# Performance work log

Measured on AMD Instinct MI355X. Metric: run time of the kernel, lower is better.

Reference implementation:

```python
import jax, jax.numpy as jnp
import numpy as np

IN_FEATURES = 4096
PADDED = 4096               # padded_dim == in_features -> no crop
K_HALF = PADDED // 2 + 1    # 2049
K = 1024                    # truncation: only first K half-spectrum coeffs active
BATCH = 8192


def setup_inputs() -> dict:
    key = jax.random.key(0)
    k1, k2, k3, k4 = jax.random.split(key, 4)
    x = jax.random.normal(k1, (BATCH, IN_FEATURES), dtype=jnp.float32)
    w_real = jax.random.normal(k2, (K_HALF,), dtype=jnp.float32) * 0.1
    w_imag = jax.random.normal(k3, (K_HALF,), dtype=jnp.float32) * 0.1
    # DC and Nyquist bins must be real (Hermitian spectrum of a real filter)
    w_imag = w_imag.at[0].set(0.0).at[-1].set(0.0)
    bias = jax.random.normal(k4, (), dtype=jnp.float32) * 0.1
    return {"x": x, "w_real": w_real, "w_imag": w_imag, "bias": bias}


def _fft_full(w_real, w_imag):
    # K-truncated half spectrum -> full Hermitian-symmetric spectrum (PADDED even)
    mask = (jnp.arange(K_HALF) < K).astype(w_real.dtype)
    half = w_real * mask + 1j * (w_imag * mask)            # (K_HALF,) complex
    nyq = half[-1].real[None].astype(half.dtype)           # real Nyquist bin
    full = jnp.concatenate([half[:-1], nyq, jnp.conj(half[1:-1])[::-1]])
    return full                                            # (PADDED,) complex


def reference(x, w_real, w_imag, bias):
    # in_features == padded_dim: no padding, no crop
    fft_full = _fft_full(w_real, w_imag)
    Xf = jnp.fft.fft(x, axis=-1, norm="ortho")             # (B, PADDED) complex
    y = jnp.fft.ifft(Xf * fft_full, axis=-1, norm="ortho").real
    return y + bias                                        # scalar bias (vector_bias=False)
```

## Files before the change

kernel.cpp:

```cpp
#include <hip/hip_runtime.h>

#define NT 256


template<bool INV>
__device__ __forceinline__ void dft16(float* vr, float* vi) {
    constexpr float C1 = 0.9238795325112867f;
    constexpr float S1 = 0.3826834323650898f;
    constexpr float HF = 0.7071067811865476f;
    const float WR[10] = {1.f,  C1,  HF,  S1, 0.f, 0.f, -HF, 0.f, 0.f, -C1};
    const float WI[10] = {0.f, -S1, -HF, -C1, -1.f, 0.f, -HF, 0.f, 0.f,  S1};

    float ar[16], ai[16];
    #pragma unroll
    for (int jl = 0; jl < 4; ++jl) {
        float x0r = vr[jl],      x0i = vi[jl];
        float x1r = vr[jl + 4],  x1i = vi[jl + 4];
        float x2r = vr[jl + 8],  x2i = vi[jl + 8];
        float x3r = vr[jl + 12], x3i = vi[jl + 12];
        float t0r = x0r + x2r, t0i = x0i + x2i;
        float t1r = x0r - x2r, t1i = x0i - x2i;
        float t2r = x1r + x3r, t2i = x1i + x3i;
        float t3r = x1r - x3r, t3i = x1i - x3i;
        ar[jl]     = t0r + t2r;  ai[jl]     = t0i + t2i;
        ar[jl + 8] = t0r - t2r;  ai[jl + 8] = t0i - t2i;
        if (!INV) {
            ar[jl + 4]  = t1r + t3i;  ai[jl + 4]  = t1i - t3r;
            ar[jl + 12] = t1r - t3i;  ai[jl + 12] = t1i + t3r;
        } else {
            ar[jl + 4]  = t1r - t3i;  ai[jl + 4]  = t1i + t3r;
            ar[jl + 12] = t1r + t3i;  ai[jl + 12] = t1i - t3r;
        }
    }
    #pragma unroll
    for (int k4 = 1; k4 < 4; ++k4) {
        #pragma unroll
        for (int jl = 1; jl < 4; ++jl) {
            const int e = jl * k4;
            float wr = WR[e];
            float wi = INV ? -WI[e] : WI[e];
            const int id = jl + 4 * k4;
            float xr = ar[id], xi = ai[id];
            ar[id] = xr * wr - xi * wi;
            ai[id] = xr * wi + xi * wr;
        }
    }
    #pragma unroll
    for (int k4 = 0; k4 < 4; ++k4) {
        float x0r = ar[4*k4 + 0], x0i = ai[4*k4 + 0];
        float x1r = ar[4*k4 + 1], x1i = ai[4*k4 + 1];
        float x2r = ar[4*k4 + 2], x2i = ai[4*k4 + 2];
        float x3r = ar[4*k4 + 3], x3i = ai[4*k4 + 3];
        float t0r = x0r + x2r, t0i = x0i + x2i;
        float t1r = x0r - x2r, t1i = x0i - x2i;
        float t2r = x1r + x3r, t2i = x1i + x3i;
        float t3r = x1r - x3r, t3i = x1i - x3i;
        vr[k4]     = t0r + t2r;  vi[k4]     = t0i + t2i;
        vr[k4 + 8] = t0r - t2r;  vi[k4 + 8] = t0i - t2i;
        if (!INV) {
            vr[k4 + 4]  = t1r + t3i;  vi[k4 + 4]  = t1i - t3r;
            vr[k4 + 12] = t1r - t3i;  vi[k4 + 12] = t1i + t3r;
        } else {
            vr[k4 + 4]  = t1r - t3i;  vi[k4 + 4]  = t1i + t3r;
            vr[k4 + 12] = t1r + t3i;  vi[k4 + 12] = t1i - t3r;
        }
    }
}

__device__ __forceinline__ void apply_tw_powers(float* vr, float* vi, float wr, float wi) {
    const float w2r = wr * wr - wi * wi;
    const float w2i = 2.0f * wr * wi;
    float aor = wr,  aoi = wi;
    float aer = w2r, aei = w2i;
    #pragma unroll
    for (int e = 1; e < 16; e += 2) {
        { float xr = vr[e], xi = vi[e];
          vr[e] = xr * aor - xi * aoi;
          vi[e] = xr * aoi + xi * aor; }
        if (e + 1 < 16) {
            float xr = vr[e + 1], xi = vi[e + 1];
            vr[e + 1] = xr * aer - xi * aei;
            vi[e + 1] = xr * aei + xi * aer;
        }
        if (e + 2 < 16) {
            float nr = aor * w2r - aoi * w2i, ni = aor * w2i + aoi * w2r;
            aor = nr; aoi = ni;
            nr = aer * w2r - aei * w2i; ni = aer * w2i + aei * w2r;
            aer = nr; aei = ni;
        }
    }
}

__global__ __launch_bounds__(NT, 4) void spectral_circulant_r16v5(
    const float* __restrict__ x,
    const float* __restrict__ w_real,
    const float* __restrict__ w_imag,
    const float* __restrict__ bias_p,
    float* __restrict__ out)
{
    __shared__ __align__(16) float2 lds[4096];

    const int t   = threadIdx.x;
    const int blk = blockIdx.x;

    float vr[16], vi[16];

    const float* __restrict__ xa = x + (size_t)(2 * blk) * 4096;
    const float* __restrict__ xb = xa + 4096;
    #pragma unroll
    for (int j = 0; j < 16; ++j) {
        vr[j] = xa[(j << 8) + t];
        vi[j] = xb[(j << 8) + t];
    }

    dft16<false>(vr, vi);
    float sA, cA;
    __sincosf((float)t * -1.5339807878856412e-3f, &sA, &cA);
    apply_tw_powers(vr, vi, cA, sA);

    {
        const int tswz = t ^ ((t >> 3) & 0xE);
        #pragma unroll
        for (int a = 0; a < 16; ++a)
            lds[(a << 8) + tswz] = make_float2(vr[a], vi[a]);
    }
    __syncthreads();

    const int ax = t >> 4;
    const int m2 = t & 15;

    int swzbase[8];
    #pragma unroll
    for (int c = 0; c < 8; ++c)
        swzbase[c] = (ax << 8) + (m2 ^ (c << 1));

    #pragma unroll
    for (int q = 0; q < 16; ++q) {
        float2 v = lds[swzbase[q & 7] + (q << 4)];
        vr[q] = v.x; vi[q] = v.y;
    }

    dft16<false>(vr, vi);
    float sB, cB;
    __sincosf((float)m2 * -2.454369260617026e-2f, &sB, &cB);
    apply_tw_powers(vr, vi, cB, sB);

    #pragma unroll
    for (int b = 0; b < 16; ++b)
        lds[swzbase[b & 7] + (b << 4)] = make_float2(vr[b], vi[b]);
    __builtin_amdgcn_wave_barrier();

    const int c2 = (m2 & 7) << 1;
    const float2* __restrict__ pbase = &lds[(ax << 8) + (m2 << 4)];
    #pragma unroll
    for (int m = 0; m < 16; m += 2) {
        float4 v = *(const float4*)&pbase[m ^ c2];
        vr[m] = v.x;     vi[m] = v.y;
        vr[m + 1] = v.z; vi[m + 1] = v.w;
    }

    dft16<false>(vr, vi);

    {
        const int c = (m2 << 4) | ax;
        const float sc = 1.0f / 4096.0f;
        #pragma unroll
        for (int r3 = 0; r3 < 4; ++r3) {
            const int k = (r3 << 8) + c;
            float hr = w_real[k] * sc;
            float hi = w_imag[k] * sc;
            float xr = vr[r3], xi = vi[r3];
            vr[r3] = xr * hr - xi * hi;
            vi[r3] = xr * hi + xi * hr;
        }
        #pragma unroll
        for (int r3 = 4; r3 < 12; ++r3) {
            vr[r3] = 0.0f; vi[r3] = 0.0f;
        }
        {
            const int idx = 1024 - c;
            const float m = (c > 0) ? sc : 0.0f;
            float hr = w_real[idx] * m;
            float hi = -w_imag[idx] * m;
            float xr = vr[12], xi = vi[12];
            vr[12] = xr * hr - xi * hi;
            vi[12] = xr * hi + xi * hr;
        }
        #pragma unroll
        for (int r3 = 13; r3 < 16; ++r3) {
            const int idx = ((16 - r3) << 8) - c;
            float hr = w_real[idx] * sc;
            float hi = -w_imag[idx] * sc;
            float xr = vr[r3], xi = vi[r3];
            vr[r3] = xr * hr - xi * hi;
            vi[r3] = xr * hi + xi * hr;
        }
    }


    dft16<true>(vr, vi);

    {
        float2* __restrict__ pw = &lds[(ax << 8) + (m2 << 4)];
        #pragma unroll
        for (int m = 0; m < 16; m += 2)
            *(float4*)&pw[m ^ c2] = make_float4(vr[m], vi[m], vr[m + 1], vi[m + 1]);
    }
    __builtin_amdgcn_wave_barrier();

    #pragma unroll
    for (int b = 0; b < 16; ++b) {
        float2 v = lds[swzbase[b & 7] + (b << 4)];
        vr[b] = v.x; vi[b] = v.y;
    }

    apply_tw_powers(vr, vi, cB, -sB);
    dft16<true>(vr, vi);

    #pragma unroll
    for (int q = 0; q < 16; ++q)
        lds[swzbase[q & 7] + (q << 4)] = make_float2(vr[q], vi[q]);
    __syncthreads();

    {
        const int tswz = t ^ ((t >> 3) & 0xE);
        #pragma unroll
        for (int a = 0; a < 16; ++a) {
            float2 v = lds[(a << 8) + tswz];
            vr[a] = v.x; vi[a] = v.y;
        }
    }

    apply_tw_powers(vr, vi, cA, -sA);
    dft16<true>(vr, vi);

    const float bv = bias_p[0];
    float* __restrict__ oa = out + (size_t)(2 * blk) * 4096;
    float* __restrict__ ob = oa + 4096;
    #pragma unroll
    for (int j = 0; j < 16; ++j) {
        __builtin_nontemporal_store(vr[j] + bv, &oa[(j << 8) + t]);
        __builtin_nontemporal_store(vi[j] + bv, &ob[(j << 8) + t]);
    }
}

extern "C" void kernel_launch(void* const* d_in, const int* in_sizes, int n_in,
                              void* d_out, int out_size, void* d_ws, size_t ws_size,
                              hipStream_t stream) {
    (void)in_sizes; (void)n_in; (void)d_ws; (void)ws_size; (void)out_size;
    const float* x      = (const float*)d_in[0];
    const float* w_real = (const float*)d_in[1];
    const float* w_imag = (const float*)d_in[2];
    const float* bias   = (const float*)d_in[3];
    float* out = (float*)d_out;

    spectral_circulant_r16v5<<<8192 / 2, NT, 0, stream>>>(x, w_real, w_imag, bias, out);
}
```

Before: 242.0 us.

## Process four rows per block as two complex FFTs per thread

Each block now handles four input rows, packed as two complex 4096-point FFTs (P and Q) per thread instead of one. Twiddle factors, weight loads and sincos work are shared across both transforms, and each thread has more independent instruction streams to hide latency. The cost is double the LDS per block (64 KB), more registers, and a lower launch-bounds occupancy target of 2 blocks per CU. The grid is halved to match.

```diff
diff --git a/kernel.cpp b/kernel.cpp
--- a/kernel.cpp
+++ b/kernel.cpp
@@ -67,20 +67,28 @@
     }
 }
 
-__device__ __forceinline__ void apply_tw_powers(float* vr, float* vi, float wr, float wi) {
+__device__ __forceinline__ void apply_tw_dual(float* vrP, float* viP,
+                                              float* vrQ, float* viQ,
+                                              float wr, float wi) {
     const float w2r = wr * wr - wi * wi;
     const float w2i = 2.0f * wr * wi;
     float aor = wr,  aoi = wi;
     float aer = w2r, aei = w2i;
     #pragma unroll
     for (int e = 1; e < 16; e += 2) {
-        { float xr = vr[e], xi = vi[e];
-          vr[e] = xr * aor - xi * aoi;
-          vi[e] = xr * aoi + xi * aor; }
+        { float xr = vrP[e], xi = viP[e];
+          vrP[e] = xr * aor - xi * aoi;
+          viP[e] = xr * aoi + xi * aor; }
+        { float xr = vrQ[e], xi = viQ[e];
+          vrQ[e] = xr * aor - xi * aoi;
+          viQ[e] = xr * aoi + xi * aor; }
         if (e + 1 < 16) {
-            float xr = vr[e + 1], xi = vi[e + 1];
-            vr[e + 1] = xr * aer - xi * aei;
-            vi[e + 1] = xr * aei + xi * aer;
+            { float xr = vrP[e + 1], xi = viP[e + 1];
+              vrP[e + 1] = xr * aer - xi * aei;
+              viP[e + 1] = xr * aei + xi * aer; }
+            { float xr = vrQ[e + 1], xi = viQ[e + 1];
+              vrQ[e + 1] = xr * aer - xi * aei;
+              viQ[e + 1] = xr * aei + xi * aer; }
         }
         if (e + 2 < 16) {
             float nr = aor * w2r - aoi * w2i, ni = aor * w2i + aoi * w2r;
@@ -91,38 +99,49 @@
     }
 }
 
-__global__ __launch_bounds__(NT, 4) void spectral_circulant_r16v5(
+__device__ __forceinline__ void cmul(float& r, float& i, float hr, float hi) {
+    float xr = r, xi = i;
+    r = xr * hr - xi * hi;
+    i = xr * hi + xi * hr;
+}
+
+__global__ __launch_bounds__(NT, 2) void spectral_circulant_r16v6(
     const float* __restrict__ x,
     const float* __restrict__ w_real,
     const float* __restrict__ w_imag,
     const float* __restrict__ bias_p,
     float* __restrict__ out)
 {
-    __shared__ __align__(16) float2 lds[4096];
+    __shared__ __align__(16) float2 lds[8192];
 
     const int t   = threadIdx.x;
     const int blk = blockIdx.x;
 
-    float vr[16], vi[16];
-
-    const float* __restrict__ xa = x + (size_t)(2 * blk) * 4096;
-    const float* __restrict__ xb = xa + 4096;
+    float vrP[16], viP[16], vrQ[16], viQ[16];
+
+    const float* __restrict__ xa = x + (size_t)(4 * blk) * 4096;
     #pragma unroll
     for (int j = 0; j < 16; ++j) {
-        vr[j] = xa[(j << 8) + t];
-        vi[j] = xb[(j << 8) + t];
-    }
-
-    dft16<false>(vr, vi);
+        const int o = (j << 8) + t;
+        vrP[j] = xa[o];
+        viP[j] = xa[o + 4096];
+        vrQ[j] = xa[o + 8192];
+        viQ[j] = xa[o + 12288];
+    }
+
+    dft16<false>(vrP, viP);
+    dft16<false>(vrQ, viQ);
     float sA, cA;
     __sincosf((float)t * -1.5339807878856412e-3f, &sA, &cA);
-    apply_tw_powers(vr, vi, cA, sA);
+    apply_tw_dual(vrP, viP, vrQ, viQ, cA, sA);
 
     {
         const int tswz = t ^ ((t >> 3) & 0xE);
         #pragma unroll
-        for (int a = 0; a < 16; ++a)
-            lds[(a << 8) + tswz] = make_float2(vr[a], vi[a]);
+        for (int a = 0; a < 16; ++a) {
+            lds[(a << 8) + tswz]        = make_float2(vrP[a], viP[a]);
+            lds[(a << 8) + tswz + 4096] = make_float2(vrQ[a], viQ[a]);
+        }
     }
     __syncthreads();
 
@@ -136,30 +155,39 @@
 
     #pragma unroll
     for (int q = 0; q < 16; ++q) {
-        float2 v = lds[swzbase[q & 7] + (q << 4)];
-        vr[q] = v.x; vi[q] = v.y;
-    }
-
-    dft16<false>(vr, vi);
+        float2 vP = lds[swzbase[q & 7] + (q << 4)];
+        float2 vQ = lds[swzbase[q & 7] + (q << 4) + 4096];
+        vrP[q] = vP.x; viP[q] = vP.y;
+        vrQ[q] = vQ.x; viQ[q] = vQ.y;
+    }
+
+    dft16<false>(vrP, viP);
+    dft16<false>(vrQ, viQ);
     float sB, cB;
     __sincosf((float)m2 * -2.454369260617026e-2f, &sB, &cB);
-    apply_tw_powers(vr, vi, cB, sB);
-
-    #pragma unroll
-    for (int b = 0; b < 16; ++b)
-        lds[swzbase[b & 7] + (b << 4)] = make_float2(vr[b], vi[b]);
+    apply_tw_dual(vrP, viP, vrQ, viQ, cB, sB);
+
+    #pragma unroll
+    for (int b = 0; b < 16; ++b) {
+        lds[swzbase[b & 7] + (b << 4)]        = make_float2(vrP[b], viP[b]);
+        lds[swzbase[b & 7] + (b << 4) + 4096] = make_float2(vrQ[b], viQ[b]);
+    }
     __builtin_amdgcn_wave_barrier();
 
     const int c2 = (m2 & 7) << 1;
     const float2* __restrict__ pbase = &lds[(ax << 8) + (m2 << 4)];
     #pragma unroll
     for (int m = 0; m < 16; m += 2) {
-        float4 v = *(const float4*)&pbase[m ^ c2];
-        vr[m] = v.x;     vi[m] = v.y;
-        vr[m + 1] = v.z; vi[m + 1] = v.w;
-    }
-
-    dft16<false>(vr, vi);
+        float4 vP = *(const float4*)&pbase[m ^ c2];
+        float4 vQ = *(const float4*)&pbase[(m ^ c2) + 4096];
+        vrP[m] = vP.x;     viP[m] = vP.y;
+        vrP[m + 1] = vP.z; viP[m + 1] = vP.w;
+        vrQ[m] = vQ.x;     viQ[m] = vQ.y;
+        vrQ[m + 1] = vQ.z; viQ[m + 1] = vQ.w;
+    }
+
+    dft16<false>(vrP, viP);
+    dft16<false>(vrQ, viQ);
 
     {
         const int c = (m2 << 4) | ax;
@@ -169,78 +197,89 @@
             const int k = (r3 << 8) + c;
             float hr = w_real[k] * sc;
             float hi = w_imag[k] * sc;
-            float xr = vr[r3], xi = vi[r3];
-            vr[r3] = xr * hr - xi * hi;
-            vi[r3] = xr * hi + xi * hr;
+            cmul(vrP[r3], viP[r3], hr, hi);
+            cmul(vrQ[r3], viQ[r3], hr, hi);
         }
         #pragma unroll
         for (int r3 = 4; r3 < 12; ++r3) {
-            vr[r3] = 0.0f; vi[r3] = 0.0f;
+            vrP[r3] = 0.0f; viP[r3] = 0.0f;
+            vrQ[r3] = 0.0f; viQ[r3] = 0.0f;
         }
         {
             const int idx = 1024 - c;
-            const float m = (c > 0) ? sc : 0.0f;
-            float hr = w_real[idx] * m;
-            float hi = -w_imag[idx] * m;
-            float xr = vr[12], xi = vi[12];
-            vr[12] = xr * hr - xi * hi;
-            vi[12] = xr * hi + xi * hr;
+            const float mm = (c > 0) ? sc : 0.0f;
+            float hr = w_real[idx] * mm;
+            float hi = -w_imag[idx] * mm;
+            cmul(vrP[12], viP[12], hr, hi);
+            cmul(vrQ[12], viQ[12], hr, hi);
         }
         #pragma unroll
         for (int r3 = 13; r3 < 16; ++r3) {
             const int idx = ((16 - r3) << 8) - c;
             float hr = w_real[idx] * sc;
             float hi = -w_imag[idx] * sc;
-            float xr = vr[r3], xi = vi[r3];
-            vr[r3] = xr * hr - xi * hi;
-            vi[r3] = xr * hi + xi * hr;
-        }
-    }
-
-
-    dft16<true>(vr, vi);
+            cmul(vrP[r3], viP[r3], hr, hi);
+            cmul(vrQ[r3], viQ[r3], hr, hi);
+        }
+    }
+
+
+    dft16<true>(vrP, viP);
+    dft16<true>(vrQ, viQ);
 
     {
         float2* __restrict__ pw = &lds[(ax << 8) + (m2 << 4)];
         #pragma unroll
-        for (int m = 0; m < 16; m += 2)
-            *(float4*)&pw[m ^ c2] = make_float4(vr[m], vi[m], vr[m + 1], vi[m + 1]);
+        for (int m = 0; m < 16; m += 2) {
+            *(float4*)&pw[m ^ c2]          = make_float4(vrP[m], viP[m], vrP[m + 1], viP[m + 1]);
+            *(float4*)&pw[(m ^ c2) + 4096] = make_float4(vrQ[m], viQ[m], vrQ[m + 1], viQ[m + 1]);
+        }
     }
     __builtin_amdgcn_wave_barrier();
 
     #pragma unroll
     for (int b = 0; b < 16; ++b) {
-        float2 v = lds[swzbase[b & 7] + (b << 4)];
-        vr[b] = v.x; vi[b] = v.y;
-    }
-
-    apply_tw_powers(vr, vi, cB, -sB);
-    dft16<true>(vr, vi);
-
-    #pragma unroll
-    for (int q = 0; q < 16; ++q)
-        lds[swzbase[q & 7] + (q << 4)] = make_float2(vr[q], vi[q]);
+        float2 vP = lds[swzbase[b & 7] + (b << 4)];
+        float2 vQ = lds[swzbase[b & 7] + (b << 4) + 4096];
+        vrP[b] = vP.x; viP[b] = vP.y;
+        vrQ[b] = vQ.x; viQ[b] = vQ.y;
+    }
+
+    apply_tw_dual(vrP, viP, vrQ, viQ, cB, -sB);
+    dft16<true>(vrP, viP);
+    dft16<true>(vrQ, viQ);
+
+    #pragma unroll
+    for (int q = 0; q < 16; ++q) {
+        lds[swzbase[q & 7] + (q << 4)]        = make_float2(vrP[q], viP[q]);
+        lds[swzbase[q & 7] + (q << 4) + 4096] = make_float2(vrQ[q], viQ[q]);
+    }
     __syncthreads();
 
     {
         const int tswz = t ^ ((t >> 3) & 0xE);
         #pragma unroll
         for (int a = 0; a < 16; ++a) {
-            float2 v = lds[(a << 8) + tswz];
-            vr[a] = v.x; vi[a] = v.y;
-        }
-    }
-
-    apply_tw_powers(vr, vi, cA, -sA);
-    dft16<true>(vr, vi);
+            float2 vP = lds[(a << 8) + tswz];
+            float2 vQ = lds[(a << 8) + tswz + 4096];
+            vrP[a] = vP.x; viP[a] = vP.y;
+            vrQ[a] = vQ.x; viQ[a] = vQ.y;
+        }
+    }
+
+    apply_tw_dual(vrP, viP, vrQ, viQ, cA, -sA);
+    dft16<true>(vrP, viP);
+    dft16<true>(vrQ, viQ);
 
     const float bv = bias_p[0];
-    float* __restrict__ oa = out + (size_t)(2 * blk) * 4096;
-    float* __restrict__ ob = oa + 4096;
+    float* __restrict__ oa = out + (size_t)(4 * blk) * 4096;
     #pragma unroll
     for (int j = 0; j < 16; ++j) {
-        __builtin_nontemporal_store(vr[j] + bv, &oa[(j << 8) + t]);
-        __builtin_nontemporal_store(vi[j] + bv, &ob[(j << 8) + t]);
+        const int o = (j << 8) + t;
+        __builtin_nontemporal_store(vrP[j] + bv, &oa[o]);
+        __builtin_nontemporal_store(viP[j] + bv, &oa[o + 4096]);
+        __builtin_nontemporal_store(vrQ[j] + bv, &oa[o + 8192]);
+        __builtin_nontemporal_store(viQ[j] + bv, &oa[o + 12288]);
     }
 }
 
@@ -254,5 +293,5 @@
     const float* bias   = (const float*)d_in[3];
     float* out = (float*)d_out;
 
-    spectral_circulant_r16v5<<<8192 / 2, NT, 0, stream>>>(x, w_real, w_imag, bias, out);
-}
+    spectral_circulant_r16v6<<<8192 / 4, NT, 0, stream>>>(x, w_real, w_imag, bias, out);
+}
```

Result: slower. 248.7 us (+2.8%).

## Process four rows per block using packed float2 vector arithmetic

Applied to the files above, without the earlier changes.

Each block now handles four input rows instead of two by packing two complex FFTs into v2f vector lanes. This lets the compiler use packed FP32 instructions (v_pk_fma/v_pk_mul) and halves the block count. LDS is split into separate real and imaginary arrays of v2f, doubling shared memory to 64 KB per block, and launch bounds drop to 2 blocks per CU. The gain in arithmetic throughput comes at the cost of more registers and lower occupancy, which may hurt latency hiding for this memory-bound kernel.

```diff
diff --git a/kernel.cpp b/kernel.cpp
--- a/kernel.cpp
+++ b/kernel.cpp
@@ -3,25 +3,28 @@
 #define NT 256
 
 
+typedef float v2f __attribute__((ext_vector_type(2)));
+typedef float v4f __attribute__((ext_vector_type(4)));
+
 template<bool INV>
-__device__ __forceinline__ void dft16(float* vr, float* vi) {
+__device__ __forceinline__ void dft16(v2f* vr, v2f* vi) {
     constexpr float C1 = 0.9238795325112867f;
     constexpr float S1 = 0.3826834323650898f;
     constexpr float HF = 0.7071067811865476f;
     const float WR[10] = {1.f,  C1,  HF,  S1, 0.f, 0.f, -HF, 0.f, 0.f, -C1};
     const float WI[10] = {0.f, -S1, -HF, -C1, -1.f, 0.f, -HF, 0.f, 0.f,  S1};
 
-    float ar[16], ai[16];
+    v2f ar[16], ai[16];
     #pragma unroll
     for (int jl = 0; jl < 4; ++jl) {
-        float x0r = vr[jl],      x0i = vi[jl];
-        float x1r = vr[jl + 4],  x1i = vi[jl + 4];
-        float x2r = vr[jl + 8],  x2i = vi[jl + 8];
-        float x3r = vr[jl + 12], x3i = vi[jl + 12];
-        float t0r = x0r + x2r, t0i = x0i + x2i;
-        float t1r = x0r - x2r, t1i = x0i - x2i;
-        float t2r = x1r + x3r, t2i = x1i + x3i;
-        float t3r = x1r - x3r, t3i = x1i - x3i;
+        v2f x0r = vr[jl],      x0i = vi[jl];
+        v2f x1r = vr[jl + 4],  x1i = vi[jl + 4];
+        v2f x2r = vr[jl + 8],  x2i = vi[jl + 8];
+        v2f x3r = vr[jl + 12], x3i = vi[jl + 12];
+        v2f t0r = x0r + x2r, t0i = x0i + x2i;
+        v2f t1r = x0r - x2r, t1i = x0i - x2i;
+        v2f t2r = x1r + x3r, t2i = x1i + x3i;
+        v2f t3r = x1r - x3r, t3i = x1i - x3i;
         ar[jl]     = t0r + t2r;  ai[jl]     = t0i + t2i;
         ar[jl + 8] = t0r - t2r;  ai[jl + 8] = t0i - t2i;
         if (!INV) {
@@ -37,24 +40,24 @@
         #pragma unroll
         for (int jl = 1; jl < 4; ++jl) {
             const int e = jl * k4;
-            float wr = WR[e];
-            float wi = INV ? -WI[e] : WI[e];
+            const float wr = WR[e];
+            const float wi = INV ? -WI[e] : WI[e];
             const int id = jl + 4 * k4;
-            float xr = ar[id], xi = ai[id];
+            v2f xr = ar[id], xi = ai[id];
             ar[id] = xr * wr - xi * wi;
             ai[id] = xr * wi + xi * wr;
         }
     }
     #pragma unroll
     for (int k4 = 0; k4 < 4; ++k4) {
-        float x0r = ar[4*k4 + 0], x0i = ai[4*k4 + 0];
-        float x1r = ar[4*k4 + 1], x1i = ai[4*k4 + 1];
-        float x2r = ar[4*k4 + 2], x2i = ai[4*k4 + 2];
-        float x3r = ar[4*k4 + 3], x3i = ai[4*k4 + 3];
-        float t0r = x0r + x2r, t0i = x0i + x2i;
-        float t1r = x0r - x2r, t1i = x0i - x2i;
-        float t2r = x1r + x3r, t2i = x1i + x3i;
-        float t3r = x1r - x3r, t3i = x1i - x3i;
+        v2f x0r = ar[4*k4 + 0], x0i = ai[4*k4 + 0];
+        v2f x1r = ar[4*k4 + 1], x1i = ai[4*k4 + 1];
+        v2f x2r = ar[4*k4 + 2], x2i = ai[4*k4 + 2];
+        v2f x3r = ar[4*k4 + 3], x3i = ai[4*k4 + 3];
+        v2f t0r = x0r + x2r, t0i = x0i + x2i;
+        v2f t1r = x0r - x2r, t1i = x0i - x2i;
+        v2f t2r = x1r + x3r, t2i = x1i + x3i;
+        v2f t3r = x1r - x3r, t3i = x1i - x3i;
         vr[k4]     = t0r + t2r;  vi[k4]     = t0i + t2i;
         vr[k4 + 8] = t0r - t2r;  vi[k4 + 8] = t0i - t2i;
         if (!INV) {
@@ -67,18 +70,18 @@
     }
 }
 
-__device__ __forceinline__ void apply_tw_powers(float* vr, float* vi, float wr, float wi) {
+__device__ __forceinline__ void apply_tw(v2f* vr, v2f* vi, float wr, float wi) {
     const float w2r = wr * wr - wi * wi;
     const float w2i = 2.0f * wr * wi;
     float aor = wr,  aoi = wi;
     float aer = w2r, aei = w2i;
     #pragma unroll
     for (int e = 1; e < 16; e += 2) {
-        { float xr = vr[e], xi = vi[e];
+        { v2f xr = vr[e], xi = vi[e];
           vr[e] = xr * aor - xi * aoi;
           vi[e] = xr * aoi + xi * aor; }
         if (e + 1 < 16) {
-            float xr = vr[e + 1], xi = vi[e + 1];
+            v2f xr = vr[e + 1], xi = vi[e + 1];
             vr[e + 1] = xr * aer - xi * aei;
             vi[e + 1] = xr * aei + xi * aer;
         }
@@ -91,38 +94,47 @@
     }
 }
 
-__global__ __launch_bounds__(NT, 4) void spectral_circulant_r16v5(
+__device__ __forceinline__ void cmul(v2f& r, v2f& i, float hr, float hi) {
+    v2f xr = r, xi = i;
+    r = xr * hr - xi * hi;
+    i = xr * hi + xi * hr;
+}
+
+__global__ __launch_bounds__(NT, 2) void spectral_circulant_r16v7(
     const float* __restrict__ x,
     const float* __restrict__ w_real,
     const float* __restrict__ w_imag,
     const float* __restrict__ bias_p,
     float* __restrict__ out)
 {
-    __shared__ __align__(16) float2 lds[4096];
+    __shared__ __align__(16) v2f ldsR[4096];
+    __shared__ __align__(16) v2f ldsI[4096];
 
     const int t   = threadIdx.x;
     const int blk = blockIdx.x;
 
-    float vr[16], vi[16];
-
-    const float* __restrict__ xa = x + (size_t)(2 * blk) * 4096;
-    const float* __restrict__ xb = xa + 4096;
+    v2f vr[16], vi[16];
+
+    const float* __restrict__ xa = x + (size_t)(4 * blk) * 4096;
     #pragma unroll
     for (int j = 0; j < 16; ++j) {
-        vr[j] = xa[(j << 8) + t];
-        vi[j] = xb[(j << 8) + t];
+        const int o = (j << 8) + t;
+        vr[j] = (v2f){xa[o],        xa[o + 8192]};
+        vi[j] = (v2f){xa[o + 4096], xa[o + 12288]};
     }
 
     dft16<false>(vr, vi);
     float sA, cA;
     __sincosf((float)t * -1.5339807878856412e-3f, &sA, &cA);
-    apply_tw_powers(vr, vi, cA, sA);
+    apply_tw(vr, vi, cA, sA);
 
     {
         const int tswz = t ^ ((t >> 3) & 0xE);
         #pragma unroll
-        for (int a = 0; a < 16; ++a)
-            lds[(a << 8) + tswz] = make_float2(vr[a], vi[a]);
+        for (int a = 0; a < 16; ++a) {
+            ldsR[(a << 8) + tswz] = vr[a];
+            ldsI[(a << 8) + tswz] = vi[a];
+        }
     }
     __syncthreads();
 
@@ -136,27 +148,30 @@
 
     #pragma unroll
     for (int q = 0; q < 16; ++q) {
-        float2 v = lds[swzbase[q & 7] + (q << 4)];
-        vr[q] = v.x; vi[q] = v.y;
+        vr[q] = ldsR[swzbase[q & 7] + (q << 4)];
+        vi[q] = ldsI[swzbase[q & 7] + (q << 4)];
     }
 
     dft16<false>(vr, vi);
     float sB, cB;
     __sincosf((float)m2 * -2.454369260617026e-2f, &sB, &cB);
-    apply_tw_powers(vr, vi, cB, sB);
-
-    #pragma unroll
-    for (int b = 0; b < 16; ++b)
-        lds[swzbase[b & 7] + (b << 4)] = make_float2(vr[b], vi[b]);
+    apply_tw(vr, vi, cB, sB);
+
+    #pragma unroll
+    for (int b = 0; b < 16; ++b) {
+        ldsR[swzbase[b & 7] + (b << 4)] = vr[b];
+        ldsI[swzbase[b & 7] + (b << 4)] = vi[b];
+    }
     __builtin_amdgcn_wave_barrier();
 
     const int c2 = (m2 & 7) << 1;
-    const float2* __restrict__ pbase = &lds[(ax << 8) + (m2 << 4)];
+    const int l0 = (ax << 8) + (m2 << 4);
     #pragma unroll
     for (int m = 0; m < 16; m += 2) {
-        float4 v = *(const float4*)&pbase[m ^ c2];
-        vr[m] = v.x;     vi[m] = v.y;
-        vr[m + 1] = v.z; vi[m + 1] = v.w;
+        v4f r4 = *(const v4f*)&ldsR[l0 + (m ^ c2)];
+        v4f i4 = *(const v4f*)&ldsI[l0 + (m ^ c2)];
+        vr[m] = r4.xy;  vr[m + 1] = r4.zw;
+        vi[m] = i4.xy;  vi[m + 1] = i4.zw;
     }
 
     dft16<false>(vr, vi);
@@ -167,80 +182,75 @@
         #pragma unroll
         for (int r3 = 0; r3 < 4; ++r3) {
             const int k = (r3 << 8) + c;
-            float hr = w_real[k] * sc;
-            float hi = w_imag[k] * sc;
-            float xr = vr[r3], xi = vi[r3];
-            vr[r3] = xr * hr - xi * hi;
-            vi[r3] = xr * hi + xi * hr;
+            cmul(vr[r3], vi[r3], w_real[k] * sc, w_imag[k] * sc);
         }
         #pragma unroll
         for (int r3 = 4; r3 < 12; ++r3) {
-            vr[r3] = 0.0f; vi[r3] = 0.0f;
+            vr[r3] = (v2f){0.0f, 0.0f};
+            vi[r3] = (v2f){0.0f, 0.0f};
         }
         {
             const int idx = 1024 - c;
-            const float m = (c > 0) ? sc : 0.0f;
-            float hr = w_real[idx] * m;
-            float hi = -w_imag[idx] * m;
-            float xr = vr[12], xi = vi[12];
-            vr[12] = xr * hr - xi * hi;
-            vi[12] = xr * hi + xi * hr;
+            const float mm = (c > 0) ? sc : 0.0f;
+            cmul(vr[12], vi[12], w_real[idx] * mm, -w_imag[idx] * mm);
         }
         #pragma unroll
         for (int r3 = 13; r3 < 16; ++r3) {
             const int idx = ((16 - r3) << 8) - c;
-            float hr = w_real[idx] * sc;
-            float hi = -w_imag[idx] * sc;
-            float xr = vr[r3], xi = vi[r3];
-            vr[r3] = xr * hr - xi * hi;
-            vi[r3] = xr * hi + xi * hr;
+            cmul(vr[r3], vi[r3], w_real[idx] * sc, -w_imag[idx] * sc);
         }
     }
 
 
     dft16<true>(vr, vi);
 
-    {
-        float2* __restrict__ pw = &lds[(ax << 8) + (m2 << 4)];
-        #pragma unroll
-        for (int m = 0; m < 16; m += 2)
-            *(float4*)&pw[m ^ c2] = make_float4(vr[m], vi[m], vr[m + 1], vi[m + 1]);
+    #pragma unroll
+    for (int m = 0; m < 16; m += 2) {
+        v4f r4, i4;
+        r4.xy = vr[m];  r4.zw = vr[m + 1];
+        i4.xy = vi[m];  i4.zw = vi[m + 1];
+        *(v4f*)&ldsR[l0 + (m ^ c2)] = r4;
+        *(v4f*)&ldsI[l0 + (m ^ c2)] = i4;
     }
     __builtin_amdgcn_wave_barrier();
 
     #pragma unroll
     for (int b = 0; b < 16; ++b) {
-        float2 v = lds[swzbase[b & 7] + (b << 4)];
-        vr[b] = v.x; vi[b] = v.y;
-    }
-
-    apply_tw_powers(vr, vi, cB, -sB);
+        vr[b] = ldsR[swzbase[b & 7] + (b << 4)];
+        vi[b] = ldsI[swzbase[b & 7] + (b << 4)];
+    }
+
+    apply_tw(vr, vi, cB, -sB);
     dft16<true>(vr, vi);
 
     #pragma unroll
-    for (int q = 0; q < 16; ++q)
-        lds[swzbase[q & 7] + (q << 4)] = make_float2(vr[q], vi[q]);
+    for (int q = 0; q < 16; ++q) {
+        ldsR[swzbase[q & 7] + (q << 4)] = vr[q];
+        ldsI[swzbase[q & 7] + (q << 4)] = vi[q];
+    }
     __syncthreads();
 
     {
         const int tswz = t ^ ((t >> 3) & 0xE);
         #pragma unroll
         for (int a = 0; a < 16; ++a) {
-            float2 v = lds[(a << 8) + tswz];
-            vr[a] = v.x; vi[a] = v.y;
-        }
-    }
-
-    apply_tw_powers(vr, vi, cA, -sA);
+            vr[a] = ldsR[(a << 8) + tswz];
+            vi[a] = ldsI[(a << 8) + tswz];
+        }
+    }
+
+    apply_tw(vr, vi, cA, -sA);
     dft16<true>(vr, vi);
 
     const float bv = bias_p[0];
-    float* __restrict__ oa = out + (size_t)(2 * blk) * 4096;
-    float* __restrict__ ob = oa + 4096;
+    float* __restrict__ oa = out + (size_t)(4 * blk) * 4096;
     #pragma unroll
     for (int j = 0; j < 16; ++j) {
-        __builtin_nontemporal_store(vr[j] + bv, &oa[(j << 8) + t]);
-        __builtin_nontemporal_store(vi[j] + bv, &ob[(j << 8) + t]);
+        const int o = (j << 8) + t;
+        __builtin_nontemporal_store(vr[j].x + bv, &oa[o]);
+        __builtin_nontemporal_store(vi[j].x + bv, &oa[o + 4096]);
+        __builtin_nontemporal_store(vr[j].y + bv, &oa[o + 8192]);
+        __builtin_nontemporal_store(vi[j].y + bv, &oa[o + 12288]);
     }
 }
 
@@ -254,5 +264,5 @@
     const float* bias   = (const float*)d_in[3];
     float* out = (float*)d_out;
 
-    spectral_circulant_r16v5<<<8192 / 2, NT, 0, stream>>>(x, w_real, w_imag, bias, out);
-}
+    spectral_circulant_r16v7<<<8192 / 4, NT, 0, stream>>>(x, w_real, w_imag, bias, out);
+}
```

Result: no change. 243.6 us (+0.6%).

## Process two row-pairs per block with software prefetch of the next input

Applied to the files above, without the earlier changes.

Each block now handles two pairs of rows (grid halved to 2048 blocks). The second pair's global loads are issued partway through the first pair's FFT pipeline, so they overlap with compute. Filter coefficients and twiddle seeds are loaded once per block and reused across both units. The cost is 32 extra live registers for the prefetch buffer, which may lower occupancy or cause spills under the 4-wave launch bound, and fewer blocks means less latency hiding across blocks.

```diff
diff --git a/kernel.cpp b/kernel.cpp
--- a/kernel.cpp
+++ b/kernel.cpp
@@ -91,7 +91,126 @@
     }
 }
 
-__global__ __launch_bounds__(NT, 4) void spectral_circulant_r16v5(
+template<bool PRE>
+__device__ __forceinline__ void process_unit(
+    float2* lds, const int t, const int ax, const int m2,
+    const int (&swzbase)[8], const int c2,
+    const float cA, const float sA, const float cB, const float sB,
+    const float (&hR)[8], const float (&hI)[8], const float bv,
+    float (&vr)[16], float (&vi)[16],
+    float (&pr)[16], float (&pi)[16],
+    const float* __restrict__ xnext,
+    float* __restrict__ oa)
+{
+    dft16<false>(vr, vi);
+    apply_tw_powers(vr, vi, cA, sA);
+
+    {
+        const int tswz = t ^ ((t >> 3) & 0xE);
+        #pragma unroll
+        for (int a = 0; a < 16; ++a)
+            lds[(a << 8) + tswz] = make_float2(vr[a], vi[a]);
+    }
+    __syncthreads();
+
+    #pragma unroll
+    for (int q = 0; q < 16; ++q) {
+        float2 v = lds[swzbase[q & 7] + (q << 4)];
+        vr[q] = v.x; vi[q] = v.y;
+    }
+
+    dft16<false>(vr, vi);
+    apply_tw_powers(vr, vi, cB, sB);
+
+    #pragma unroll
+    for (int b = 0; b < 16; ++b)
+        lds[swzbase[b & 7] + (b << 4)] = make_float2(vr[b], vi[b]);
+    __builtin_amdgcn_wave_barrier();
+
+    const float2* __restrict__ pbase = &lds[(ax << 8) + (m2 << 4)];
+    #pragma unroll
+    for (int m = 0; m < 16; m += 2) {
+        float4 v = *(const float4*)&pbase[m ^ c2];
+        vr[m] = v.x;     vi[m] = v.y;
+        vr[m + 1] = v.z; vi[m + 1] = v.w;
+    }
+
+    if constexpr (PRE) {
+        #pragma unroll
+        for (int j = 0; j < 16; ++j) {
+            pr[j] = xnext[(j << 8) + t];
+            pi[j] = xnext[(j << 8) + t + 4096];
+        }
+    }
+
+    dft16<false>(vr, vi);
+
+    {
+        #pragma unroll
+        for (int r3 = 0; r3 < 4; ++r3) {
+            float xr = vr[r3], xi = vi[r3];
+            vr[r3] = xr * hR[r3] - xi * hI[r3];
+            vi[r3] = xr * hI[r3] + xi * hR[r3];
+        }
+        #pragma unroll
+        for (int r3 = 4; r3 < 12; ++r3) { vr[r3] = 0.0f; vi[r3] = 0.0f; }
+        {
+            float xr = vr[12], xi = vi[12];
+            vr[12] = xr * hR[4] - xi * hI[4];
+            vi[12] = xr * hI[4] + xi * hR[4];
+        }
+        #pragma unroll
+        for (int r3 = 13; r3 < 16; ++r3) {
+            float xr = vr[r3], xi = vi[r3];
+            vr[r3] = xr * hR[r3 - 8] - xi * hI[r3 - 8];
+            vi[r3] = xr * hI[r3 - 8] + xi * hR[r3 - 8];
+        }
+    }
+
+    dft16<true>(vr, vi);
+
+    {
+        float2* __restrict__ pw = &lds[(ax << 8) + (m2 << 4)];
+        #pragma unroll
+        for (int m = 0; m < 16; m += 2)
+            *(float4*)&pw[m ^ c2] = make_float4(vr[m], vi[m], vr[m + 1], vi[m + 1]);
+    }
+    __builtin_amdgcn_wave_barrier();
+
+    #pragma unroll
+    for (int b = 0; b < 16; ++b) {
+        float2 v = lds[swzbase[b & 7] + (b << 4)];
+        vr[b] = v.x; vi[b] = v.y;
+    }
+
+    apply_tw_powers(vr, vi, cB, -sB);
+    dft16<true>(vr, vi);
+
+    #pragma unroll
+    for (int q = 0; q < 16; ++q)
+        lds[swzbase[q & 7] + (q << 4)] = make_float2(vr[q], vi[q]);
+    __syncthreads();
+
+    {
+        const int tswz = t ^ ((t >> 3) & 0xE);
+        #pragma unroll
+        for (int a = 0; a < 16; ++a) {
+            float2 v = lds[(a << 8) + tswz];
+            vr[a] = v.x; vi[a] = v.y;
+        }
+    }
+
+    apply_tw_powers(vr, vi, cA, -sA);
+    dft16<true>(vr, vi);
+
+    #pragma unroll
+    for (int j = 0; j < 16; ++j) {
+        __builtin_nontemporal_store(vr[j] + bv, &oa[(j << 8) + t]);
+        __builtin_nontemporal_store(vi[j] + bv, &oa[(j << 8) + t + 4096]);
+    }
+}
+
+__global__ __launch_bounds__(NT, 4) void spectral_circulant_r16v8(
     const float* __restrict__ x,
     const float* __restrict__ w_real,
     const float* __restrict__ w_imag,
@@ -102,146 +221,62 @@
 
     const int t   = threadIdx.x;
     const int blk = blockIdx.x;
-
-    float vr[16], vi[16];
-
-    const float* __restrict__ xa = x + (size_t)(2 * blk) * 4096;
-    const float* __restrict__ xb = xa + 4096;
-    #pragma unroll
-    for (int j = 0; j < 16; ++j) {
-        vr[j] = xa[(j << 8) + t];
-        vi[j] = xb[(j << 8) + t];
-    }
-
-    dft16<false>(vr, vi);
-    float sA, cA;
-    __sincosf((float)t * -1.5339807878856412e-3f, &sA, &cA);
-    apply_tw_powers(vr, vi, cA, sA);
-
-    {
-        const int tswz = t ^ ((t >> 3) & 0xE);
-        #pragma unroll
-        for (int a = 0; a < 16; ++a)
-            lds[(a << 8) + tswz] = make_float2(vr[a], vi[a]);
-    }
-    __syncthreads();
-
-    const int ax = t >> 4;
-    const int m2 = t & 15;
+    const int ax  = t >> 4;
+    const int m2  = t & 15;
 
     int swzbase[8];
     #pragma unroll
     for (int c = 0; c < 8; ++c)
         swzbase[c] = (ax << 8) + (m2 ^ (c << 1));
-
-    #pragma unroll
-    for (int q = 0; q < 16; ++q) {
-        float2 v = lds[swzbase[q & 7] + (q << 4)];
-        vr[q] = v.x; vi[q] = v.y;
-    }
-
-    dft16<false>(vr, vi);
-    float sB, cB;
+    const int c2 = (m2 & 7) << 1;
+
+    float sA, cA, sB, cB;
+    __sincosf((float)t  * -1.5339807878856412e-3f, &sA, &cA);
     __sincosf((float)m2 * -2.454369260617026e-2f, &sB, &cB);
-    apply_tw_powers(vr, vi, cB, sB);
-
-    #pragma unroll
-    for (int b = 0; b < 16; ++b)
-        lds[swzbase[b & 7] + (b << 4)] = make_float2(vr[b], vi[b]);
-    __builtin_amdgcn_wave_barrier();
-
-    const int c2 = (m2 & 7) << 1;
-    const float2* __restrict__ pbase = &lds[(ax << 8) + (m2 << 4)];
-    #pragma unroll
-    for (int m = 0; m < 16; m += 2) {
-        float4 v = *(const float4*)&pbase[m ^ c2];
-        vr[m] = v.x;     vi[m] = v.y;
-        vr[m + 1] = v.z; vi[m + 1] = v.w;
-    }
-
-    dft16<false>(vr, vi);
-
+
+    float hR[8], hI[8];
     {
         const int c = (m2 << 4) | ax;
         const float sc = 1.0f / 4096.0f;
         #pragma unroll
         for (int r3 = 0; r3 < 4; ++r3) {
-            const int k = (r3 << 8) + c;
-            float hr = w_real[k] * sc;
-            float hi = w_imag[k] * sc;
-            float xr = vr[r3], xi = vi[r3];
-            vr[r3] = xr * hr - xi * hi;
-            vi[r3] = xr * hi + xi * hr;
-        }
-        #pragma unroll
-        for (int r3 = 4; r3 < 12; ++r3) {
-            vr[r3] = 0.0f; vi[r3] = 0.0f;
+            hR[r3] = w_real[(r3 << 8) + c] * sc;
+            hI[r3] = w_imag[(r3 << 8) + c] * sc;
         }
         {
             const int idx = 1024 - c;
-            const float m = (c > 0) ? sc : 0.0f;
-            float hr = w_real[idx] * m;
-            float hi = -w_imag[idx] * m;
-            float xr = vr[12], xi = vi[12];
-            vr[12] = xr * hr - xi * hi;
-            vi[12] = xr * hi + xi * hr;
+            const float mm = (c > 0) ? sc : 0.0f;
+            hR[4] = w_real[idx] * mm;
+            hI[4] = -w_imag[idx] * mm;
         }
         #pragma unroll
         for (int r3 = 13; r3 < 16; ++r3) {
             const int idx = ((16 - r3) << 8) - c;
-            float hr = w_real[idx] * sc;
-            float hi = -w_imag[idx] * sc;
-            float xr = vr[r3], xi = vi[r3];
-            vr[r3] = xr * hr - xi * hi;
-            vi[r3] = xr * hi + xi * hr;
-        }
-    }
-
-
-    dft16<true>(vr, vi);
-
-    {
-        float2* __restrict__ pw = &lds[(ax << 8) + (m2 << 4)];
-        #pragma unroll
-        for (int m = 0; m < 16; m += 2)
-            *(float4*)&pw[m ^ c2] = make_float4(vr[m], vi[m], vr[m + 1], vi[m + 1]);
-    }
-    __builtin_amdgcn_wave_barrier();
-
-    #pragma unroll
-    for (int b = 0; b < 16; ++b) {
-        float2 v = lds[swzbase[b & 7] + (b << 4)];
-        vr[b] = v.x; vi[b] = v.y;
-    }
-
-    apply_tw_powers(vr, vi, cB, -sB);
-    dft16<true>(vr, vi);
-
-    #pragma unroll
-    for (int q = 0; q < 16; ++q)
-        lds[swzbase[q & 7] + (q << 4)] = make_float2(vr[q], vi[q]);
+            hR[r3 - 8] = w_real[idx] * sc;
+            hI[r3 - 8] = -w_imag[idx] * sc;
+        }
+    }
+    const float bv = bias_p[0];
+
+    float vrA[16], viA[16], vrB[16], viB[16];
+    const float* __restrict__ xa0 = x + (size_t)(2 * blk) * 4096;
+    const float* __restrict__ xa1 = x + (size_t)(2 * (blk + 2048)) * 4096;
+    float* __restrict__ oa0 = out + (size_t)(2 * blk) * 4096;
+    float* __restrict__ oa1 = out + (size_t)(2 * (blk + 2048)) * 4096;
+
+    #pragma unroll
+    for (int j = 0; j < 16; ++j) {
+        vrA[j] = xa0[(j << 8) + t];
+        viA[j] = xa0[(j << 8) + t + 4096];
+    }
+
+    process_unit<true>(lds, t, ax, m2, swzbase, c2, cA, sA, cB, sB,
+                       hR, hI, bv, vrA, viA, vrB, viB, xa1, oa0);
+
     __syncthreads();
 
-    {
-        const int tswz = t ^ ((t >> 3) & 0xE);
-        #pragma unroll
-        for (int a = 0; a < 16; ++a) {
-            float2 v = lds[(a << 8) + tswz];
-            vr[a] = v.x; vi[a] = v.y;
-        }
-    }
-
-    apply_tw_powers(vr, vi, cA, -sA);
-    dft16<true>(vr, vi);
-
-    const float bv = bias_p[0];
-    float* __restrict__ oa = out + (size_t)(2 * blk) * 4096;
-    float* __restrict__ ob = oa + 4096;
-    #pragma unroll
-    for (int j = 0; j < 16; ++j) {
-        __builtin_nontemporal_store(vr[j] + bv, &oa[(j << 8) + t]);
-        __builtin_nontemporal_store(vi[j] + bv, &ob[(j << 8) + t]);
-    }
+    process_unit<false>(lds, t, ax, m2, swzbase, c2, cA, sA, cB, sB,
+                        hR, hI, bv, vrB, viB, vrA, viA, nullptr, oa1);
 }
 
 extern "C" void kernel_launch(void* const* d_in, const int* in_sizes, int n_in,
@@ -254,5 +289,5 @@
     const float* bias   = (const float*)d_in[3];
     float* out = (float*)d_out;
 
-    spectral_circulant_r16v5<<<8192 / 2, NT, 0, stream>>>(x, w_real, w_imag, bias, out);
-}
+    spectral_circulant_r16v8<<<2048, NT, 0, stream>>>(x, w_real, w_imag, bias, out);
+}
```

Result: slower. 358.6 us (+48.1%).
